# Optimization experiments

Hardware: AMD Instinct MI355X
Metric: run time of the kernel (lower is better)

Reference implementation:

```python
import jax, jax.numpy as jnp
import numpy as np

B, N, C = 16, 2048, 384
CLUSTER_NUM = 512
K_NN = 5


def setup_inputs() -> dict:
    key = jax.random.key(0)
    k1, k2, k3, k4 = jax.random.split(key, 4)
    x = jax.random.normal(k1, (B, N, C), dtype=jnp.float32)
    idx_token = jax.random.randint(k2, (B, N), 0, N)
    agg_weight = jnp.ones((B, N, 1), dtype=jnp.float32)
    density_noise = jax.random.uniform(k3, (B, N), dtype=jnp.float32)
    score_w = jax.random.normal(k4, (1, C), dtype=jnp.float32) * 0.02
    score_b = jnp.zeros((1,), dtype=jnp.float32)
    return {"x": x, "idx_token": idx_token, "agg_weight": agg_weight,
            "density_noise": density_noise, "score_w": score_w, "score_b": score_b}


def _cluster_dpc_knn(x, density_noise, cluster_num, k):
    # x: [B,N,C]; clustering is done under no_grad in the original
    x = jax.lax.stop_gradient(x)
    b, n, c = x.shape
    sq = jnp.sum(x * x, axis=-1)  # [B,N]
    d2 = sq[:, :, None] + sq[:, None, :] - 2.0 * jnp.einsum('bnc,bmc->bnm', x, x)
    dist = jnp.sqrt(jnp.maximum(d2, 0.0)) / (c ** 0.5)  # [B,N,N] cdist/sqrt(C)
    # k smallest distances per row
    neg_near, _ = jax.lax.top_k(-dist, k)                # [B,N,k]
    density = jnp.exp(-jnp.mean(neg_near * neg_near, axis=-1))  # [B,N]
    density = density + density_noise * 1e-6             # tie-break noise
    mask = (density[:, None, :] > density[:, :, None]).astype(x.dtype)  # [B,N,N]
    dist_max = jnp.max(dist.reshape(b, -1), axis=-1)[:, None, None]
    dmin = jnp.min(dist * mask + dist_max * (1.0 - mask), axis=-1)  # [B,N]
    score = dmin * density
    _, index_down = jax.lax.top_k(score, cluster_num)    # [B,K] cluster centers
    dist_sub = jnp.take_along_axis(dist, index_down[:, :, None], axis=1)  # [B,K,N]
    idx_cluster = jnp.argmin(dist_sub, axis=1)           # [B,N]
    bi = jnp.arange(b)[:, None]
    centers = jnp.broadcast_to(jnp.arange(cluster_num)[None, :], (b, cluster_num))
    idx_cluster = idx_cluster.at[bi, index_down].set(centers)
    return idx_cluster, index_down


def reference(x, idx_token, agg_weight, density_noise, score_w, score_b):
    b, n, c = x.shape
    kc = CLUSTER_NUM
    # token score -> weight (equal_weight=False)
    token_weight = jnp.exp(x @ score_w.T + score_b)      # [B,N,1]
    idx_cluster, _ = _cluster_dpc_knn(x, density_noise, kc, K_NN)
    # merge tokens via segment sums
    bi = jnp.arange(b)[:, None]
    idx = (idx_cluster + bi * kc).reshape(-1)            # [B*N]
    all_weight = jax.ops.segment_sum(token_weight.reshape(-1, 1), idx,
                                     num_segments=b * kc) + 1e-6  # [B*K,1]
    norm_weight = token_weight / all_weight[idx].reshape(b, n, 1)
    x_merged = jax.ops.segment_sum((x * norm_weight).reshape(-1, c), idx,
                                   num_segments=b * kc).reshape(b, kc, c)
    idx_token_new = jnp.take_along_axis(idx_cluster, idx_token, axis=1)  # [B,N]
    weight_t = jnp.take_along_axis(norm_weight, idx_token[:, :, None], axis=1)
    agg_weight_new = agg_weight * weight_t               # [B,N,1]
    return x_merged, idx_token_new, agg_weight_new
```

## Files before the change

### kernel.cpp

```cpp
#include <hip/hip_runtime.h>
#include <math.h>

static constexpr int BB  = 16;
static constexpr int NN  = 2048;
static constexpr int CC  = 384;
static constexpr int KCL = 512;
static constexpr float RSQC = 0.051031036307982884f;

typedef short  bf16x8 __attribute__((ext_vector_type(8)));
typedef float  f32x4  __attribute__((ext_vector_type(4)));

__device__ __forceinline__ unsigned short f2b(float v) {
    unsigned u = __float_as_uint(v);
    unsigned r = (u + 0x7FFFu + ((u >> 16) & 1u)) >> 16;
    return (unsigned short)r;
}
__device__ __forceinline__ float b2f(unsigned short b) {
    return __uint_as_float(((unsigned)b) << 16);
}

__device__ __forceinline__ void gload16(const void* g, void* l) {
    __builtin_amdgcn_global_load_lds(
        (const __attribute__((address_space(1))) void*)g,
        (__attribute__((address_space(3))) void*)l, 16, 0, 0);
}

__global__ __launch_bounds__(256) void k_prep(
    const float* __restrict__ x, const float* __restrict__ sw,
    const float* __restrict__ sb, float* __restrict__ sq, float* __restrict__ tw,
    unsigned short* __restrict__ Xh, unsigned short* __restrict__ Xl)
{
    int row  = blockIdx.x * 4 + (threadIdx.x >> 6);
    int lane = threadIdx.x & 63;
    const float* xr = x + (size_t)row * CC;
    unsigned short* xh = Xh + (size_t)row * CC;
    unsigned short* xl = Xl + (size_t)row * CC;
    float s2 = 0.f, sd = 0.f;
    for (int c = lane; c < CC; c += 64) {
        float v = xr[c];
        s2 += v * v;
        sd += v * sw[c];
        unsigned short h = f2b(v);
        xh[c] = h;
        xl[c] = f2b(v - b2f(h));
    }
    #pragma unroll
    for (int o = 32; o > 0; o >>= 1) {
        s2 += __shfl_down(s2, o);
        sd += __shfl_down(sd, o);
    }
    if (lane == 0) {
        sq[row] = s2;
        tw[row] = expf(sd + sb[0]);
    }
}

__global__ __launch_bounds__(256) void k_rowstats(
    const float* __restrict__ x, const float* __restrict__ sw,
    const float* __restrict__ sb, float* __restrict__ sq, float* __restrict__ tw)
{
    int row  = blockIdx.x * 4 + (threadIdx.x >> 6);
    int lane = threadIdx.x & 63;
    const float* xr = x + (size_t)row * CC;
    float s2 = 0.f, sd = 0.f;
    for (int c = lane; c < CC; c += 64) {
        float v = xr[c];
        s2 += v * v;
        sd += v * sw[c];
    }
    #pragma unroll
    for (int o = 32; o > 0; o >>= 1) {
        s2 += __shfl_down(s2, o);
        sd += __shfl_down(sd, o);
    }
    if (lane == 0) {
        sq[row] = s2;
        tw[row] = expf(sd + sb[0]);
    }
}


__global__ __launch_bounds__(256) void k_gemm_sym(
    const unsigned short* __restrict__ Xh, const unsigned short* __restrict__ Xl,
    const float* __restrict__ sq, float* __restrict__ D, int b0)
{
    const int b = b0 + blockIdx.z;
    int q = blockIdx.x;
    int ti = 0;
    while (q >= (16 - ti)) { q -= (16 - ti); ++ti; }
    const int tj = ti + q;
    const int i0 = ti * 128, j0 = tj * 128;

    const unsigned short* Xhb = Xh + (size_t)b * NN * CC;
    const unsigned short* Xlb = Xl + (size_t)b * NN * CC;
    const float* sqb = sq + b * NN;
    float* Db = D + (size_t)blockIdx.z * NN * NN;

    __shared__ union {
        unsigned short u16[4][128][32];
        float tr[64][129];
    } sm;

    const int t  = threadIdx.x;
    const int w  = t >> 6;
    const int l  = t & 63;
    const int wr = w >> 1, wc = w & 1;
    const int lt = l & 15, sl = l >> 4;

    f32x4 acc[4][4];
    #pragma unroll
    for (int fr = 0; fr < 4; ++fr)
        #pragma unroll
        for (int fc = 0; fc < 4; ++fc) acc[fr][fc] = (f32x4)0.0f;

    for (int kc = 0; kc < CC; kc += 32) {
        #pragma unroll
        for (int p = 0; p < 4; ++p) {
            const unsigned short* src = (p == 0) ? Xhb : (p == 1) ? Xlb
                                      : (p == 2) ? Xhb : Xlb;
            const int base0 = (p < 2) ? i0 : j0;
            #pragma unroll
            for (int u = 0; u < 2; ++u) {
                int seg = w * 2 + u;
                int r   = seg * 16 + (l >> 2);
                int s   = (l & 3) ^ ((r >> 1) & 3);
                gload16(src + (size_t)(base0 + r) * CC + kc + s * 8,
                        &sm.u16[p][seg * 16][0]);
            }
        }
        __syncthreads();

        bf16x8 fah[4], fal[4], fbh[4], fbl[4];
        #pragma unroll
        for (int fr = 0; fr < 4; ++fr) {
            int ra = wr * 64 + fr * 16 + lt;
            int sa = (sl ^ ((ra >> 1) & 3)) * 8;
            fah[fr] = *(const bf16x8*)&sm.u16[0][ra][sa];
            fal[fr] = *(const bf16x8*)&sm.u16[1][ra][sa];
        }
        #pragma unroll
        for (int fc = 0; fc < 4; ++fc) {
            int rb = wc * 64 + fc * 16 + lt;
            int sb_ = (sl ^ ((rb >> 1) & 3)) * 8;
            fbh[fc] = *(const bf16x8*)&sm.u16[2][rb][sb_];
            fbl[fc] = *(const bf16x8*)&sm.u16[3][rb][sb_];
        }
        #pragma unroll
        for (int fr = 0; fr < 4; ++fr)
            #pragma unroll
            for (int fc = 0; fc < 4; ++fc) {
                acc[fr][fc] = __builtin_amdgcn_mfma_f32_16x16x32_bf16(
                    fah[fr], fbh[fc], acc[fr][fc], 0, 0, 0);
                acc[fr][fc] = __builtin_amdgcn_mfma_f32_16x16x32_bf16(
                    fah[fr], fbl[fc], acc[fr][fc], 0, 0, 0);
                acc[fr][fc] = __builtin_amdgcn_mfma_f32_16x16x32_bf16(
                    fal[fr], fbh[fc], acc[fr][fc], 0, 0, 0);
            }
        __syncthreads();
    }

    float sqr[4][4], sqc[4];
    #pragma unroll
    for (int fr = 0; fr < 4; ++fr)
        #pragma unroll
        for (int reg = 0; reg < 4; ++reg)
            sqr[fr][reg] = sqb[i0 + wr * 64 + fr * 16 + sl * 4 + reg];
    #pragma unroll
    for (int fc = 0; fc < 4; ++fc)
        sqc[fc] = sqb[j0 + wc * 64 + fc * 16 + lt];

    #pragma unroll
    for (int fr = 0; fr < 4; ++fr)
        #pragma unroll
        for (int fc = 0; fc < 4; ++fc)
            #pragma unroll
            for (int reg = 0; reg < 4; ++reg) {
                int row = i0 + wr * 64 + fr * 16 + sl * 4 + reg;
                int col = j0 + wc * 64 + fc * 16 + lt;
                float d2 = fmaxf(sqr[fr][reg] + sqc[fc] - 2.0f * acc[fr][fc][reg], 0.0f);
                Db[(size_t)row * NN + col] = d2;
            }

    if (ti != tj) {
        #pragma unroll
        for (int h = 0; h < 2; ++h) {
            __syncthreads();
            if (wr == h) {
                #pragma unroll
                for (int fr = 0; fr < 4; ++fr)
                    #pragma unroll
                    for (int fc = 0; fc < 4; ++fc)
                        #pragma unroll
                        for (int reg = 0; reg < 4; ++reg) {
                            int rl = fr * 16 + sl * 4 + reg;
                            int cl = wc * 64 + fc * 16 + lt;
                            float d2 = fmaxf(sqr[fr][reg] + sqc[fc]
                                             - 2.0f * acc[fr][fc][reg], 0.0f);
                            sm.tr[rl][cl] = d2;
                        }
            }
            __syncthreads();
            for (int idx = t; idx < 128 * 64; idx += 256) {
                int c  = idx >> 6;
                int rl = idx & 63;
                Db[(size_t)(j0 + c) * NN + i0 + h * 64 + rl] = sm.tr[rl][c];
            }
        }
    }
}

__global__ __launch_bounds__(256) void k_density2(
    const float* __restrict__ D, const float* __restrict__ noise,
    float* __restrict__ dens, float* __restrict__ rowmax)
{
    int gid  = blockIdx.x * 4 + (threadIdx.x >> 6);
    int lane = threadIdx.x & 63;
    const float* row = D + (size_t)gid * NN;
    float t5[5] = {1e30f, 1e30f, 1e30f, 1e30f, 1e30f};
    float mx = 0.f;
    auto ins5 = [&](float v) {
        if (v < t5[4]) {
            t5[4] = v;
            #pragma unroll
            for (int q = 4; q > 0; --q) {
                if (t5[q] < t5[q - 1]) { float tmp = t5[q - 1]; t5[q - 1] = t5[q]; t5[q] = tmp; }
            }
        }
    };
    #pragma unroll
    for (int it = 0; it < 8; ++it) {
        float4 v = ((const float4*)row)[it * 64 + lane];
        mx = fmaxf(mx, fmaxf(fmaxf(v.x, v.y), fmaxf(v.z, v.w)));
        ins5(v.x); ins5(v.y); ins5(v.z); ins5(v.w);
    }
    #pragma unroll
    for (int o = 1; o < 64; o <<= 1) {
        float b0 = __shfl_xor(t5[0], o), b1 = __shfl_xor(t5[1], o);
        float b2 = __shfl_xor(t5[2], o), b3 = __shfl_xor(t5[3], o);
        float b4 = __shfl_xor(t5[4], o);
        mx = fmaxf(mx, __shfl_xor(mx, o));
        ins5(b0); ins5(b1); ins5(b2); ins5(b3); ins5(b4);
    }
    if (lane == 0) {
        float m2 = (t5[0] + t5[1] + t5[2] + t5[3] + t5[4]) * (1.0f / (5.0f * CC));
        dens[gid]   = expf(-m2) + noise[gid] * 1e-6f;
        rowmax[gid] = mx;
    }
}

__global__ __launch_bounds__(256) void k_distmax2(
    const float* __restrict__ rowmax, float* __restrict__ dmax)
{
    int b = blockIdx.x, t = threadIdx.x;
    float m = 0.f;
    for (int i = t; i < NN; i += 256) m = fmaxf(m, rowmax[b * NN + i]);
    __shared__ float red[256];
    red[t] = m; __syncthreads();
    for (int o = 128; o > 0; o >>= 1) {
        if (t < o) red[t] = fmaxf(red[t], red[t + o]);
        __syncthreads();
    }
    if (t == 0) dmax[b] = sqrtf(red[0]) * RSQC;
}

__global__ __launch_bounds__(256) void k_dmin2(
    const float* __restrict__ D, const float* __restrict__ dens,
    const float* __restrict__ dmax, float* __restrict__ score)
{
    int gid  = blockIdx.x * 4 + (threadIdx.x >> 6);
    int lane = threadIdx.x & 63;
    int bl   = gid >> 11;
    const float* row = D + (size_t)gid * NN;
    const float* dn  = dens + (size_t)bl * NN;
    float di = dens[gid];
    float m = 1e30f;
    #pragma unroll
    for (int it = 0; it < 8; ++it) {
        float4 v = ((const float4*)row)[it * 64 + lane];
        float4 dj = ((const float4*)dn)[it * 64 + lane];
        if (dj.x > di) m = fminf(m, v.x);
        if (dj.y > di) m = fminf(m, v.y);
        if (dj.z > di) m = fminf(m, v.z);
        if (dj.w > di) m = fminf(m, v.w);
    }
    #pragma unroll
    for (int o = 32; o > 0; o >>= 1) m = fminf(m, __shfl_down(m, o));
    if (lane == 0) {
        float dm = fminf(sqrtf(m) * RSQC, dmax[bl]);
        score[gid] = dm * di;
    }
}

__global__ __launch_bounds__(256) void k_assign2(
    const float* __restrict__ D, const int* __restrict__ idown,
    int* __restrict__ idxc)
{
    int bl = blockIdx.y;
    int tl = threadIdx.x & 63;
    int g  = threadIdx.x >> 6;
    int n  = blockIdx.x * 64 + tl;
    const float* Db = D + (size_t)bl * NN * NN;
    const int* idb  = idown + bl * KCL;
    float best = 1e30f; int bk = 0;
    for (int k = g * 128; k < (g + 1) * 128; ++k) {
        float v = Db[(size_t)idb[k] * NN + n];
        if (v < best) { best = v; bk = k; }
    }
    __shared__ float bvs[4][64];
    __shared__ int   bks[4][64];
    bvs[g][tl] = best; bks[g][tl] = bk;
    __syncthreads();
    if (threadIdx.x < 64) {
        float bv = bvs[0][threadIdx.x]; int bkk = bks[0][threadIdx.x];
        #pragma unroll
        for (int gg = 1; gg < 4; ++gg) {
            if (bvs[gg][threadIdx.x] < bv) { bv = bvs[gg][threadIdx.x]; bkk = bks[gg][threadIdx.x]; }
        }
        idxc[bl * NN + blockIdx.x * 64 + threadIdx.x] = bkk;
    }
}


__global__ __launch_bounds__(256) void k_density(
    const float* __restrict__ x, const float* __restrict__ sq,
    const float* __restrict__ noise, float* __restrict__ dens,
    float* __restrict__ rowmax)
{
    const int b  = blockIdx.y;
    const int i0 = blockIdx.x * 64;
    const float* xb  = x + (size_t)b * NN * CC;
    const float* sqb = sq + b * NN;
    __shared__ float As[16][64];
    __shared__ float Bs[16][64];
    __shared__ float mrg[64][16][5];
    __shared__ float mrgmax[64][16];
    const int t  = threadIdx.x;
    const int tx = t & 15, ty = t >> 4;
    const int lr = t >> 2, lk4 = (t & 3) * 4;

    float top[4][5];
    float rmax[4];
    float sqi[4];
    #pragma unroll
    for (int r = 0; r < 4; ++r) {
        sqi[r]  = sqb[i0 + ty * 4 + r];
        rmax[r] = 0.f;
        #pragma unroll
        for (int q = 0; q < 5; ++q) top[r][q] = 1e30f;
    }

    for (int j0 = 0; j0 < NN; j0 += 64) {
        float acc[4][4];
        #pragma unroll
        for (int r = 0; r < 4; ++r)
            #pragma unroll
            for (int s = 0; s < 4; ++s) acc[r][s] = 0.f;

        for (int k0 = 0; k0 < CC; k0 += 16) {
            float4 av = *(const float4*)(xb + (size_t)(i0 + lr) * CC + k0 + lk4);
            float4 bv = *(const float4*)(xb + (size_t)(j0 + lr) * CC + k0 + lk4);
            As[lk4 + 0][lr] = av.x; As[lk4 + 1][lr] = av.y;
            As[lk4 + 2][lr] = av.z; As[lk4 + 3][lr] = av.w;
            Bs[lk4 + 0][lr] = bv.x; Bs[lk4 + 1][lr] = bv.y;
            Bs[lk4 + 2][lr] = bv.z; Bs[lk4 + 3][lr] = bv.w;
            __syncthreads();
            #pragma unroll
            for (int kk = 0; kk < 16; ++kk) {
                float4 a4 = *(const float4*)&As[kk][ty * 4];
                float4 b4 = *(const float4*)&Bs[kk][tx * 4];
                float ar[4] = {a4.x, a4.y, a4.z, a4.w};
                float br[4] = {b4.x, b4.y, b4.z, b4.w};
                #pragma unroll
                for (int r = 0; r < 4; ++r)
                    #pragma unroll
                    for (int s = 0; s < 4; ++s)
                        acc[r][s] = fmaf(ar[r], br[s], acc[r][s]);
            }
            __syncthreads();
        }
        float sqj[4];
        #pragma unroll
        for (int s = 0; s < 4; ++s) sqj[s] = sqb[j0 + tx * 4 + s];
        #pragma unroll
        for (int r = 0; r < 4; ++r) {
            #pragma unroll
            for (int s = 0; s < 4; ++s) {
                float d2 = sqi[r] + sqj[s] - 2.0f * acc[r][s];
                float d  = sqrtf(fmaxf(d2, 0.0f)) * RSQC;
                rmax[r] = fmaxf(rmax[r], d);
                if (d < top[r][4]) {
                    top[r][4] = d;
                    #pragma unroll
                    for (int q = 4; q > 0; --q) {
                        if (top[r][q] < top[r][q - 1]) {
                            float tmp = top[r][q - 1];
                            top[r][q - 1] = top[r][q];
                            top[r][q] = tmp;
                        }
                    }
                }
            }
        }
    }
    #pragma unroll
    for (int r = 0; r < 4; ++r) {
        #pragma unroll
        for (int q = 0; q < 5; ++q) mrg[ty * 4 + r][tx][q] = top[r][q];
        mrgmax[ty * 4 + r][tx] = rmax[r];
    }
    __syncthreads();
    if (t < 64) {
        float t5[5] = {1e30f, 1e30f, 1e30f, 1e30f, 1e30f};
        float mx = 0.f;
        for (int c = 0; c < 16; ++c) {
            mx = fmaxf(mx, mrgmax[t][c]);
            #pragma unroll
            for (int q = 0; q < 5; ++q) {
                float d = mrg[t][c][q];
                if (d < t5[4]) {
                    t5[4] = d;
                    #pragma unroll
                    for (int u = 4; u > 0; --u) {
                        if (t5[u] < t5[u - 1]) {
                            float tmp = t5[u - 1]; t5[u - 1] = t5[u]; t5[u] = tmp;
                        }
                    }
                }
            }
        }
        float m2 = (t5[0]*t5[0] + t5[1]*t5[1] + t5[2]*t5[2] +
                    t5[3]*t5[3] + t5[4]*t5[4]) / 5.0f;
        int i = i0 + t;
        dens[b * NN + i]   = expf(-m2) + noise[b * NN + i] * 1e-6f;
        rowmax[b * NN + i] = mx;
    }
}

__global__ __launch_bounds__(256) void k_distmax(
    const float* __restrict__ rowmax, float* __restrict__ dmax)
{
    int b = blockIdx.x, t = threadIdx.x;
    float m = 0.f;
    for (int i = t; i < NN; i += 256) m = fmaxf(m, rowmax[b * NN + i]);
    __shared__ float red[256];
    red[t] = m; __syncthreads();
    for (int o = 128; o > 0; o >>= 1) {
        if (t < o) red[t] = fmaxf(red[t], red[t + o]);
        __syncthreads();
    }
    if (t == 0) dmax[b] = red[0];
}

__global__ __launch_bounds__(256) void k_dmin(
    const float* __restrict__ x, const float* __restrict__ sq,
    const float* __restrict__ dens, const float* __restrict__ dmax,
    float* __restrict__ score)
{
    const int b  = blockIdx.y;
    const int i0 = blockIdx.x * 64;
    const float* xb  = x + (size_t)b * NN * CC;
    const float* sqb = sq + b * NN;
    const float* dnb = dens + b * NN;
    __shared__ float As[16][64];
    __shared__ float Bs[16][64];
    __shared__ float mrgmin[64][16];
    const int t  = threadIdx.x;
    const int tx = t & 15, ty = t >> 4;
    const int lr = t >> 2, lk4 = (t & 3) * 4;

    float sqi[4], di[4], mn[4];
    #pragma unroll
    for (int r = 0; r < 4; ++r) {
        sqi[r] = sqb[i0 + ty * 4 + r];
        di[r]  = dnb[i0 + ty * 4 + r];
        mn[r]  = 1e30f;
    }

    for (int j0 = 0; j0 < NN; j0 += 64) {
        float acc[4][4];
        #pragma unroll
        for (int r = 0; r < 4; ++r)
            #pragma unroll
            for (int s = 0; s < 4; ++s) acc[r][s] = 0.f;

        for (int k0 = 0; k0 < CC; k0 += 16) {
            float4 av = *(const float4*)(xb + (size_t)(i0 + lr) * CC + k0 + lk4);
            float4 bv = *(const float4*)(xb + (size_t)(j0 + lr) * CC + k0 + lk4);
            As[lk4 + 0][lr] = av.x; As[lk4 + 1][lr] = av.y;
            As[lk4 + 2][lr] = av.z; As[lk4 + 3][lr] = av.w;
            Bs[lk4 + 0][lr] = bv.x; Bs[lk4 + 1][lr] = bv.y;
            Bs[lk4 + 2][lr] = bv.z; Bs[lk4 + 3][lr] = bv.w;
            __syncthreads();
            #pragma unroll
            for (int kk = 0; kk < 16; ++kk) {
                float4 a4 = *(const float4*)&As[kk][ty * 4];
                float4 b4 = *(const float4*)&Bs[kk][tx * 4];
                float ar[4] = {a4.x, a4.y, a4.z, a4.w};
                float br[4] = {b4.x, b4.y, b4.z, b4.w};
                #pragma unroll
                for (int r = 0; r < 4; ++r)
                    #pragma unroll
                    for (int s = 0; s < 4; ++s)
                        acc[r][s] = fmaf(ar[r], br[s], acc[r][s]);
            }
            __syncthreads();
        }
        float dj[4];
        #pragma unroll
        for (int s = 0; s < 4; ++s) dj[s] = dnb[j0 + tx * 4 + s];
        float sqj[4];
        #pragma unroll
        for (int s = 0; s < 4; ++s) sqj[s] = sqb[j0 + tx * 4 + s];
        #pragma unroll
        for (int r = 0; r < 4; ++r) {
            #pragma unroll
            for (int s = 0; s < 4; ++s) {
                float d2 = sqi[r] + sqj[s] - 2.0f * acc[r][s];
                float d  = sqrtf(fmaxf(d2, 0.0f)) * RSQC;
                if (dj[s] > di[r]) mn[r] = fminf(mn[r], d);
            }
        }
    }
    #pragma unroll
    for (int r = 0; r < 4; ++r) mrgmin[ty * 4 + r][tx] = mn[r];
    __syncthreads();
    if (t < 64) {
        float m = 1e30f;
        for (int c = 0; c < 16; ++c) m = fminf(m, mrgmin[t][c]);
        float dm = fminf(dmax[b], m);
        score[b * NN + i0 + t] = dm * dnb[i0 + t];
    }
}

__global__ __launch_bounds__(256) void k_assign(
    const float* __restrict__ x, const float* __restrict__ sq,
    const int* __restrict__ idown, int* __restrict__ idxc)
{
    const int b  = blockIdx.y;
    const int n0 = blockIdx.x * 64;
    const float* xb  = x + (size_t)b * NN * CC;
    const float* sqb = sq + b * NN;
    const int* idb = idown + b * KCL;
    __shared__ float As[16][64];
    __shared__ float Bs[16][64];
    __shared__ float mv[64][16];
    __shared__ int   mk[64][16];
    const int t  = threadIdx.x;
    const int tx = t & 15, ty = t >> 4;
    const int lr = t >> 2, lk4 = (t & 3) * 4;

    float sqt[4];
    #pragma unroll
    for (int s = 0; s < 4; ++s) sqt[s] = sqb[n0 + tx * 4 + s];
    float bestv[4] = {1e30f, 1e30f, 1e30f, 1e30f};
    int   bestk[4] = {0, 0, 0, 0};

    for (int c0 = 0; c0 < KCL; c0 += 64) {
        int crow = idb[c0 + lr];
        float acc[4][4];
        #pragma unroll
        for (int r = 0; r < 4; ++r)
            #pragma unroll
            for (int s = 0; s < 4; ++s) acc[r][s] = 0.f;

        for (int k0 = 0; k0 < CC; k0 += 16) {
            float4 av = *(const float4*)(xb + (size_t)crow * CC + k0 + lk4);
            float4 bv = *(const float4*)(xb + (size_t)(n0 + lr) * CC + k0 + lk4);
            As[lk4 + 0][lr] = av.x; As[lk4 + 1][lr] = av.y;
            As[lk4 + 2][lr] = av.z; As[lk4 + 3][lr] = av.w;
            Bs[lk4 + 0][lr] = bv.x; Bs[lk4 + 1][lr] = bv.y;
            Bs[lk4 + 2][lr] = bv.z; Bs[lk4 + 3][lr] = bv.w;
            __syncthreads();
            #pragma unroll
            for (int kk = 0; kk < 16; ++kk) {
                float4 a4 = *(const float4*)&As[kk][ty * 4];
                float4 b4 = *(const float4*)&Bs[kk][tx * 4];
                float ar[4] = {a4.x, a4.y, a4.z, a4.w};
                float br[4] = {b4.x, b4.y, b4.z, b4.w};
                #pragma unroll
                for (int r = 0; r < 4; ++r)
                    #pragma unroll
                    for (int s = 0; s < 4; ++s)
                        acc[r][s] = fmaf(ar[r], br[s], acc[r][s]);
            }
            __syncthreads();
        }
        float sqc[4];
        #pragma unroll
        for (int r = 0; r < 4; ++r) sqc[r] = sqb[idb[c0 + ty * 4 + r]];
        #pragma unroll
        for (int r = 0; r < 4; ++r) {
            int kg = c0 + ty * 4 + r;
            #pragma unroll
            for (int s = 0; s < 4; ++s) {
                float e = fmaxf(sqc[r] + sqt[s] - 2.0f * acc[r][s], 0.0f);
                if (e < bestv[s]) { bestv[s] = e; bestk[s] = kg; }
            }
        }
    }
    #pragma unroll
    for (int s = 0; s < 4; ++s) {
        mv[tx * 4 + s][ty] = bestv[s];
        mk[tx * 4 + s][ty] = bestk[s];
    }
    __syncthreads();
    if (t < 64) {
        float bv = 1e30f; int bk = 1 << 30;
        for (int c = 0; c < 16; ++c) {
            float v = mv[t][c]; int k = mk[t][c];
            if (v < bv || (v == bv && k < bk)) { bv = v; bk = k; }
        }
        idxc[b * NN + n0 + t] = bk;
    }
}


__global__ __launch_bounds__(1024) void k_topk(
    const float* __restrict__ score, int* __restrict__ idown)
{
    int b = blockIdx.x, t = threadIdx.x;
    __shared__ float s[NN];
    __shared__ int   si[NN];
    s[t]         = score[b * NN + t];        si[t]        = t;
    s[t + 1024]  = score[b * NN + t + 1024]; si[t + 1024] = t + 1024;
    __syncthreads();
    for (int k = 2; k <= NN; k <<= 1) {
        for (int j = k >> 1; j > 0; j >>= 1) {
            int i = (t & (j - 1)) | ((t & ~(j - 1)) << 1);
            int l = i | j;
            bool dir = ((i & k) == 0);
            float svi = s[i], svl = s[l];
            int   ii  = si[i], il = si[l];
            bool before_l_i = (svl > svi) || (svl == svi && il < ii);
            if (before_l_i == dir) {
                s[i] = svl; s[l] = svi;
                si[i] = il; si[l] = ii;
            }
            __syncthreads();
        }
    }
    if (t < KCL) idown[b * KCL + t] = si[t];
}

__global__ __launch_bounds__(256) void k_override(
    const int* __restrict__ idown, int* __restrict__ idxc)
{
    int g = blockIdx.x * 256 + threadIdx.x;
    int b = g >> 9, k = g & 511;
    idxc[b * NN + idown[g]] = k;
}

__global__ __launch_bounds__(512) void k_merge(
    const float* __restrict__ x, const float* __restrict__ tw,
    const int* __restrict__ idxc, float* __restrict__ aw, float* __restrict__ xm)
{
    int b = blockIdx.y, k = blockIdx.x;
    __shared__ int members[NN];
    __shared__ int wc[8];
    __shared__ float red[512];
    int t = threadIdx.x, lane = t & 63, w = t >> 6;
    const int* ib = idxc + b * NN;
    int base = 0;
    for (int r0 = 0; r0 < NN; r0 += 512) {
        int n = r0 + t;
        bool m = (ib[n] == k);
        unsigned long long msk = __ballot(m);
        if (lane == 0) wc[w] = __popcll(msk);
        __syncthreads();
        int off = 0;
        for (int ww = 0; ww < w; ++ww) off += wc[ww];
        int tot = 0;
        #pragma unroll
        for (int ww = 0; ww < 8; ++ww) tot += wc[ww];
        if (m) members[base + off + __popcll(msk & ((1ull << lane) - 1ull))] = n;
        base += tot;
        __syncthreads();
    }
    int cnt = base;
    const float* twb = tw + b * NN;
    float ps = 0.f;
    for (int p = t; p < cnt; p += 512) ps += twb[members[p]];
    red[t] = ps; __syncthreads();
    for (int o = 256; o > 0; o >>= 1) {
        if (t < o) red[t] += red[t + o];
        __syncthreads();
    }
    float awf = red[0] + 1e-6f;
    if (t == 0) aw[b * KCL + k] = awf;
    if (t < CC) {
        const float* xb = x + (size_t)b * NN * CC;
        float s = 0.f;
        for (int p = 0; p < cnt; ++p) {
            int n = members[p];
            s += xb[(size_t)n * CC + t] * twb[n];
        }
        xm[((size_t)b * KCL + k) * CC + t] = s / awf;
    }
}

__global__ __launch_bounds__(256) void k_out(
    const int* __restrict__ idx_token, const float* __restrict__ aggw,
    const float* __restrict__ tw, const float* __restrict__ aw,
    const int* __restrict__ idxc, float* __restrict__ out_idx,
    float* __restrict__ out_agg)
{
    int g = blockIdx.x * 256 + threadIdx.x;
    int b = g >> 11;
    int it = idx_token[g];
    int kclu = idxc[b * NN + it];
    out_idx[g] = (float)kclu;
    float nw = tw[b * NN + it] / aw[b * KCL + kclu];
    out_agg[g] = aggw[g] * nw;
}

extern "C" void kernel_launch(void* const* d_in, const int* in_sizes, int n_in,
                              void* d_out, int out_size, void* d_ws, size_t ws_size,
                              hipStream_t stream) {
    const float* x         = (const float*)d_in[0];
    const int*   idx_token = (const int*)  d_in[1];
    const float* aggw      = (const float*)d_in[2];
    const float* noise     = (const float*)d_in[3];
    const float* sw        = (const float*)d_in[4];
    const float* sb        = (const float*)d_in[5];

    float* ws      = (float*)d_ws;
    float* sq      = ws;
    float* tw      = ws + 32768;
    float* dens    = ws + 65536;
    float* rowmax  = ws + 98304;
    float* score   = ws + 131072;
    float* dmax    = ws + 163840;
    float* aw      = ws + 163904;
    int*   idown   = (int*)(ws + 172096);
    int*   idxc    = (int*)(ws + 180288);

    unsigned short* Xh = (unsigned short*)(ws + 213056);
    unsigned short* Xl = (unsigned short*)(ws + 213056 + 6291456);
    float* Dbuf        = ws + 213056 + 2 * 6291456;

    const size_t head_bytes = (size_t)(213056 + 2 * 6291456) * 4;
    size_t avail = (ws_size > head_bytes) ? (ws_size - head_bytes) : 0;
    int nbg = 0;
    for (int g = 16; g >= 1; g >>= 1) {
        if ((size_t)g * NN * NN * 4 <= avail) { nbg = g; break; }
    }

    float* xm      = (float*)d_out;
    float* out_idx = xm + (size_t)BB * KCL * CC;
    float* out_agg = out_idx + (size_t)BB * NN;

    if (nbg >= 16) {
        k_prep    <<<dim3(BB * NN / 4), 256, 0, stream>>>(x, sw, sb, sq, tw, Xh, Xl);
        k_gemm_sym<<<dim3(136, 1, BB), 256, 0, stream>>>(Xh, Xl, sq, Dbuf, 0);
        k_density2<<<dim3(BB * NN / 4), 256, 0, stream>>>(Dbuf, noise, dens, rowmax);
        k_distmax2<<<dim3(BB), 256, 0, stream>>>(rowmax, dmax);
        k_dmin2   <<<dim3(BB * NN / 4), 256, 0, stream>>>(Dbuf, dens, dmax, score);
        k_topk    <<<dim3(BB), 1024, 0, stream>>>(score, idown);
        k_assign2 <<<dim3(NN / 64, BB), 256, 0, stream>>>(Dbuf, idown, idxc);
        k_override<<<dim3(BB * KCL / 256), 256, 0, stream>>>(idown, idxc);
    } else if (nbg >= 1) {
        k_prep<<<dim3(BB * NN / 4), 256, 0, stream>>>(x, sw, sb, sq, tw, Xh, Xl);
        int G = (nbg >= 8) ? 8 : nbg;
        for (int b0 = 0; b0 < BB; b0 += G) {
            int g = (b0 + G <= BB) ? G : (BB - b0);
            k_gemm_sym<<<dim3(136, 1, g), 256, 0, stream>>>(Xh, Xl, sq, Dbuf, b0);
            k_density2<<<dim3(g * NN / 4), 256, 0, stream>>>(Dbuf, noise + b0 * NN,
                                                             dens + b0 * NN, rowmax + b0 * NN);
            k_distmax2<<<dim3(g), 256, 0, stream>>>(rowmax + b0 * NN, dmax + b0);
            k_dmin2   <<<dim3(g * NN / 4), 256, 0, stream>>>(Dbuf, dens + b0 * NN,
                                                             dmax + b0, score + b0 * NN);
            k_topk    <<<dim3(g), 1024, 0, stream>>>(score + b0 * NN, idown + b0 * KCL);
            k_assign2 <<<dim3(NN / 64, g), 256, 0, stream>>>(Dbuf, idown + b0 * KCL,
                                                             idxc + b0 * NN);
            k_override<<<dim3(g * KCL / 256), 256, 0, stream>>>(idown + b0 * KCL,
                                                                idxc + b0 * NN);
        }
    } else {
        k_rowstats<<<dim3(BB * NN / 4), 256, 0, stream>>>(x, sw, sb, sq, tw);
        k_density <<<dim3(NN / 64, BB), 256, 0, stream>>>(x, sq, noise, dens, rowmax);
        k_distmax <<<dim3(BB), 256, 0, stream>>>(rowmax, dmax);
        k_dmin    <<<dim3(NN / 64, BB), 256, 0, stream>>>(x, sq, dens, dmax, score);
        k_topk    <<<dim3(BB), 1024, 0, stream>>>(score, idown);
        k_assign  <<<dim3(NN / 64, BB), 256, 0, stream>>>(x, sq, idown, idxc);
        k_override<<<dim3(BB * KCL / 256), 256, 0, stream>>>(idown, idxc);
    }

    k_merge<<<dim3(KCL, BB), 512, 0, stream>>>(x, tw, idxc, aw, xm);
    k_out  <<<dim3(BB * NN / 256), 256, 0, stream>>>(idx_token, aggw, tw, aw, idxc,
                                                     out_idx, out_agg);
}
```

Baseline: 445.5 us.

## Fuse density top-5 and row max into symmetric distance GEMM epilogue

The GEMM epilogue now computes per-tile partial top-5 smallest distances and row/column maxima, writing them to a small partial buffer. A lighter density kernel then merges 16 tile partials instead of rescanning the full NxN distance matrix, and it atomically reduces the global distance max, removing a separate max kernel. The override kernel is folded into assign through an inverse-index map built in top-k. The change also adds nontemporal stores for D and a workgroup remap across batches. This trades extra epilogue work and shuffles in the GEMM for one fewer full pass over D.

```diff
diff --git a/kernel.cpp b/kernel.cpp
--- a/kernel.cpp
+++ b/kernel.cpp
@@ -18,18 +18,28 @@
 __device__ __forceinline__ float b2f(unsigned short b) {
     return __uint_as_float(((unsigned)b) << 16);
 }
-
 __device__ __forceinline__ void gload16(const void* g, void* l) {
     __builtin_amdgcn_global_load_lds(
         (const __attribute__((address_space(1))) void*)g,
         (__attribute__((address_space(3))) void*)l, 16, 0, 0);
 }
+__device__ __forceinline__ void ins5(float* t5, float v) {
+    if (v < t5[4]) {
+        t5[4] = v;
+        #pragma unroll
+        for (int q = 4; q > 0; --q) {
+            if (t5[q] < t5[q - 1]) { float tmp = t5[q - 1]; t5[q - 1] = t5[q]; t5[q] = tmp; }
+        }
+    }
+}
 
 __global__ __launch_bounds__(256) void k_prep(
     const float* __restrict__ x, const float* __restrict__ sw,
     const float* __restrict__ sb, float* __restrict__ sq, float* __restrict__ tw,
-    unsigned short* __restrict__ Xh, unsigned short* __restrict__ Xl)
-{
+    unsigned short* __restrict__ Xh, unsigned short* __restrict__ Xl,
+    unsigned* __restrict__ dmaxraw)
+{
+    if (blockIdx.x == 0 && threadIdx.x < 64) dmaxraw[threadIdx.x] = 0u;
     int row  = blockIdx.x * 4 + (threadIdx.x >> 6);
     int lane = threadIdx.x & 63;
     const float* xr = x + (size_t)row * CC;
@@ -82,10 +92,15 @@
 
 __global__ __launch_bounds__(256) void k_gemm_sym(
     const unsigned short* __restrict__ Xh, const unsigned short* __restrict__ Xl,
-    const float* __restrict__ sq, float* __restrict__ D, int b0)
-{
-    const int b = b0 + blockIdx.z;
-    int q = blockIdx.x;
+    const float* __restrict__ sq, float* __restrict__ D, float* __restrict__ P,
+    int b0)
+{
+    int f   = blockIdx.x + 136 * blockIdx.z;
+    int nwg = 136 * gridDim.z;
+    int wg  = ((nwg & 7) == 0) ? ((f & 7) * (nwg >> 3) + (f >> 3)) : f;
+    int bz  = wg / 136;
+    int q   = wg % 136;
+    const int b = b0 + bz;
     int ti = 0;
     while (q >= (16 - ti)) { q -= (16 - ti); ++ti; }
     const int tj = ti + q;
@@ -94,11 +109,12 @@
     const unsigned short* Xhb = Xh + (size_t)b * NN * CC;
     const unsigned short* Xlb = Xl + (size_t)b * NN * CC;
     const float* sqb = sq + b * NN;
-    float* Db = D + (size_t)blockIdx.z * NN * NN;
+    float* Db = D + (size_t)bz * NN * NN;
 
     __shared__ union {
         unsigned short u16[4][128][32];
         float tr[64][129];
+        float part[2][128][8];
     } sm;
 
     const int t  = threadIdx.x;
@@ -178,10 +194,98 @@
                 int row = i0 + wr * 64 + fr * 16 + sl * 4 + reg;
                 int col = j0 + wc * 64 + fc * 16 + lt;
                 float d2 = fmaxf(sqr[fr][reg] + sqc[fc] - 2.0f * acc[fr][fc][reg], 0.0f);
-                Db[(size_t)row * NN + col] = d2;
-            }
+                __builtin_nontemporal_store(d2, Db + (size_t)row * NN + col);
+            }
+
+    #pragma unroll
+    for (int fr = 0; fr < 4; ++fr) {
+        #pragma unroll
+        for (int reg = 0; reg < 4; ++reg) {
+            float t5[5] = {1e30f, 1e30f, 1e30f, 1e30f, 1e30f};
+            float rmx = 0.f;
+            #pragma unroll
+            for (int fc = 0; fc < 4; ++fc) {
+                float d2 = fmaxf(sqr[fr][reg] + sqc[fc] - 2.0f * acc[fr][fc][reg], 0.0f);
+                rmx = fmaxf(rmx, d2);
+                ins5(t5, d2);
+            }
+            #pragma unroll
+            for (int mk = 1; mk <= 8; mk <<= 1) {
+                float o0 = __shfl_xor(t5[0], mk), o1 = __shfl_xor(t5[1], mk);
+                float o2 = __shfl_xor(t5[2], mk), o3 = __shfl_xor(t5[3], mk);
+                float o4 = __shfl_xor(t5[4], mk);
+                rmx = fmaxf(rmx, __shfl_xor(rmx, mk));
+                ins5(t5, o0); ins5(t5, o1); ins5(t5, o2); ins5(t5, o3); ins5(t5, o4);
+            }
+            if (lt == 0) {
+                int rl = wr * 64 + fr * 16 + sl * 4 + reg;
+                sm.part[wc][rl][0] = t5[0]; sm.part[wc][rl][1] = t5[1];
+                sm.part[wc][rl][2] = t5[2]; sm.part[wc][rl][3] = t5[3];
+                sm.part[wc][rl][4] = t5[4]; sm.part[wc][rl][5] = rmx;
+            }
+        }
+    }
+    __syncthreads();
+    if (t < 128) {
+        float t5[5]; float rmx;
+        #pragma unroll
+        for (int qq = 0; qq < 5; ++qq) t5[qq] = sm.part[0][t][qq];
+        rmx = sm.part[0][t][5];
+        #pragma unroll
+        for (int qq = 0; qq < 5; ++qq) ins5(t5, sm.part[1][t][qq]);
+        rmx = fmaxf(rmx, sm.part[1][t][5]);
+        float* dst = P + ((size_t)(b * 16 + tj) * NN + (i0 + t)) * 8;
+        float4 o0 = {t5[0], t5[1], t5[2], t5[3]};
+        float4 o1 = {t5[4], rmx, 0.f, 0.f};
+        *(float4*)dst = o0;
+        *(float4*)(dst + 4) = o1;
+    }
 
     if (ti != tj) {
+        __syncthreads();
+        #pragma unroll
+        for (int fc = 0; fc < 4; ++fc) {
+            float t5[5] = {1e30f, 1e30f, 1e30f, 1e30f, 1e30f};
+            float cmx = 0.f;
+            #pragma unroll
+            for (int fr = 0; fr < 4; ++fr)
+                #pragma unroll
+                for (int reg = 0; reg < 4; ++reg) {
+                    float d2 = fmaxf(sqr[fr][reg] + sqc[fc] - 2.0f * acc[fr][fc][reg], 0.0f);
+                    cmx = fmaxf(cmx, d2);
+                    ins5(t5, d2);
+                }
+            #pragma unroll
+            for (int mk = 16; mk <= 32; mk <<= 1) {
+                float o0 = __shfl_xor(t5[0], mk), o1 = __shfl_xor(t5[1], mk);
+                float o2 = __shfl_xor(t5[2], mk), o3 = __shfl_xor(t5[3], mk);
+                float o4 = __shfl_xor(t5[4], mk);
+                cmx = fmaxf(cmx, __shfl_xor(cmx, mk));
+                ins5(t5, o0); ins5(t5, o1); ins5(t5, o2); ins5(t5, o3); ins5(t5, o4);
+            }
+            if (sl == 0) {
+                int cl = wc * 64 + fc * 16 + lt;
+                sm.part[wr][cl][0] = t5[0]; sm.part[wr][cl][1] = t5[1];
+                sm.part[wr][cl][2] = t5[2]; sm.part[wr][cl][3] = t5[3];
+                sm.part[wr][cl][4] = t5[4]; sm.part[wr][cl][5] = cmx;
+            }
+        }
+        __syncthreads();
+        if (t < 128) {
+            float t5[5]; float cmx;
+            #pragma unroll
+            for (int qq = 0; qq < 5; ++qq) t5[qq] = sm.part[0][t][qq];
+            cmx = sm.part[0][t][5];
+            #pragma unroll
+            for (int qq = 0; qq < 5; ++qq) ins5(t5, sm.part[1][t][qq]);
+            cmx = fmaxf(cmx, sm.part[1][t][5]);
+            float* dst = P + ((size_t)(b * 16 + ti) * NN + (j0 + t)) * 8;
+            float4 o0 = {t5[0], t5[1], t5[2], t5[3]};
+            float4 o1 = {t5[4], cmx, 0.f, 0.f};
+            *(float4*)dst = o0;
+            *(float4*)(dst + 4) = o1;
+        }
+
         #pragma unroll
         for (int h = 0; h < 2; ++h) {
             __syncthreads();
@@ -203,69 +307,44 @@
             for (int idx = t; idx < 128 * 64; idx += 256) {
                 int c  = idx >> 6;
                 int rl = idx & 63;
-                Db[(size_t)(j0 + c) * NN + i0 + h * 64 + rl] = sm.tr[rl][c];
-            }
-        }
-    }
-}
-
-__global__ __launch_bounds__(256) void k_density2(
-    const float* __restrict__ D, const float* __restrict__ noise,
-    float* __restrict__ dens, float* __restrict__ rowmax)
-{
-    int gid  = blockIdx.x * 4 + (threadIdx.x >> 6);
-    int lane = threadIdx.x & 63;
-    const float* row = D + (size_t)gid * NN;
+                __builtin_nontemporal_store(sm.tr[rl][c],
+                    Db + (size_t)(j0 + c) * NN + i0 + h * 64 + rl);
+            }
+        }
+    }
+}
+
+__global__ __launch_bounds__(256) void k_density3(
+    const float* __restrict__ P, const float* __restrict__ noise,
+    float* __restrict__ dens, unsigned* __restrict__ dmaxraw)
+{
+    int gid = blockIdx.x * 256 + threadIdx.x;
+    int b   = gid >> 11;
+    int n   = gid & 2047;
+    const float* p = P + ((size_t)(b * 16) * NN + n) * 8;
     float t5[5] = {1e30f, 1e30f, 1e30f, 1e30f, 1e30f};
     float mx = 0.f;
-    auto ins5 = [&](float v) {
-        if (v < t5[4]) {
-            t5[4] = v;
-            #pragma unroll
-            for (int q = 4; q > 0; --q) {
-                if (t5[q] < t5[q - 1]) { float tmp = t5[q - 1]; t5[q - 1] = t5[q]; t5[q] = tmp; }
-            }
-        }
-    };
-    #pragma unroll
-    for (int it = 0; it < 8; ++it) {
-        float4 v = ((const float4*)row)[it * 64 + lane];
-        mx = fmaxf(mx, fmaxf(fmaxf(v.x, v.y), fmaxf(v.z, v.w)));
-        ins5(v.x); ins5(v.y); ins5(v.z); ins5(v.w);
-    }
-    #pragma unroll
-    for (int o = 1; o < 64; o <<= 1) {
-        float b0 = __shfl_xor(t5[0], o), b1 = __shfl_xor(t5[1], o);
-        float b2 = __shfl_xor(t5[2], o), b3 = __shfl_xor(t5[3], o);
-        float b4 = __shfl_xor(t5[4], o);
-        mx = fmaxf(mx, __shfl_xor(mx, o));
-        ins5(b0); ins5(b1); ins5(b2); ins5(b3); ins5(b4);
-    }
-    if (lane == 0) {
-        float m2 = (t5[0] + t5[1] + t5[2] + t5[3] + t5[4]) * (1.0f / (5.0f * CC));
-        dens[gid]   = expf(-m2) + noise[gid] * 1e-6f;
-        rowmax[gid] = mx;
-    }
-}
-
-__global__ __launch_bounds__(256) void k_distmax2(
-    const float* __restrict__ rowmax, float* __restrict__ dmax)
-{
-    int b = blockIdx.x, t = threadIdx.x;
-    float m = 0.f;
-    for (int i = t; i < NN; i += 256) m = fmaxf(m, rowmax[b * NN + i]);
+    #pragma unroll
+    for (int tc = 0; tc < 16; ++tc) {
+        float4 a = *(const float4*)(p + (size_t)tc * NN * 8);
+        float4 c = *(const float4*)(p + (size_t)tc * NN * 8 + 4);
+        ins5(t5, a.x); ins5(t5, a.y); ins5(t5, a.z); ins5(t5, a.w); ins5(t5, c.x);
+        mx = fmaxf(mx, c.y);
+    }
+    float m2 = (t5[0] + t5[1] + t5[2] + t5[3] + t5[4]) * (1.0f / (5.0f * CC));
+    dens[gid] = expf(-m2) + noise[gid] * 1e-6f;
     __shared__ float red[256];
-    red[t] = m; __syncthreads();
+    red[threadIdx.x] = mx; __syncthreads();
     for (int o = 128; o > 0; o >>= 1) {
-        if (t < o) red[t] = fmaxf(red[t], red[t + o]);
+        if (threadIdx.x < o) red[threadIdx.x] = fmaxf(red[threadIdx.x], red[threadIdx.x + o]);
         __syncthreads();
     }
-    if (t == 0) dmax[b] = sqrtf(red[0]) * RSQC;
+    if (threadIdx.x == 0) atomicMax(&dmaxraw[b], __float_as_uint(red[0]));
 }
 
 __global__ __launch_bounds__(256) void k_dmin2(
     const float* __restrict__ D, const float* __restrict__ dens,
-    const float* __restrict__ dmax, float* __restrict__ score)
+    const unsigned* __restrict__ dmaxraw, float* __restrict__ score)
 {
     int gid  = blockIdx.x * 4 + (threadIdx.x >> 6);
     int lane = threadIdx.x & 63;
@@ -276,7 +355,7 @@
     float m = 1e30f;
     #pragma unroll
     for (int it = 0; it < 8; ++it) {
-        float4 v = ((const float4*)row)[it * 64 + lane];
+        float4 v  = ((const float4*)row)[it * 64 + lane];
         float4 dj = ((const float4*)dn)[it * 64 + lane];
         if (dj.x > di) m = fminf(m, v.x);
         if (dj.y > di) m = fminf(m, v.y);
@@ -286,14 +365,15 @@
     #pragma unroll
     for (int o = 32; o > 0; o >>= 1) m = fminf(m, __shfl_down(m, o));
     if (lane == 0) {
-        float dm = fminf(sqrtf(m) * RSQC, dmax[bl]);
+        float dmv = sqrtf(__uint_as_float(dmaxraw[bl])) * RSQC;
+        float dm = fminf(sqrtf(m) * RSQC, dmv);
         score[gid] = dm * di;
     }
 }
 
 __global__ __launch_bounds__(256) void k_assign2(
     const float* __restrict__ D, const int* __restrict__ idown,
-    int* __restrict__ idxc)
+    const int* __restrict__ invc, int* __restrict__ idxc)
 {
     int bl = blockIdx.y;
     int tl = threadIdx.x & 63;
@@ -316,7 +396,9 @@
         for (int gg = 1; gg < 4; ++gg) {
             if (bvs[gg][threadIdx.x] < bv) { bv = bvs[gg][threadIdx.x]; bkk = bks[gg][threadIdx.x]; }
         }
-        idxc[bl * NN + blockIdx.x * 64 + threadIdx.x] = bkk;
+        int nn = blockIdx.x * 64 + threadIdx.x;
+        int iv = invc[bl * NN + nn];
+        idxc[bl * NN + nn] = (iv >= 0) ? iv : bkk;
     }
 }
 
@@ -415,18 +497,7 @@
         for (int c = 0; c < 16; ++c) {
             mx = fmaxf(mx, mrgmax[t][c]);
             #pragma unroll
-            for (int q = 0; q < 5; ++q) {
-                float d = mrg[t][c][q];
-                if (d < t5[4]) {
-                    t5[4] = d;
-                    #pragma unroll
-                    for (int u = 4; u > 0; --u) {
-                        if (t5[u] < t5[u - 1]) {
-                            float tmp = t5[u - 1]; t5[u - 1] = t5[u]; t5[u] = tmp;
-                        }
-                    }
-                }
-            }
+            for (int q = 0; q < 5; ++q) ins5(t5, mrg[t][c][q]);
         }
         float m2 = (t5[0]*t5[0] + t5[1]*t5[1] + t5[2]*t5[2] +
                     t5[3]*t5[3] + t5[4]*t5[4]) / 5.0f;
@@ -614,9 +685,17 @@
     }
 }
 
+__global__ __launch_bounds__(256) void k_override(
+    const int* __restrict__ idown, int* __restrict__ idxc)
+{
+    int g = blockIdx.x * 256 + threadIdx.x;
+    int b = g >> 9, k = g & 511;
+    idxc[b * NN + idown[g]] = k;
+}
+
 
 __global__ __launch_bounds__(1024) void k_topk(
-    const float* __restrict__ score, int* __restrict__ idown)
+    const float* __restrict__ score, int* __restrict__ idown, int* __restrict__ invc)
 {
     int b = blockIdx.x, t = threadIdx.x;
     __shared__ float s[NN];
@@ -640,14 +719,10 @@
         }
     }
     if (t < KCL) idown[b * KCL + t] = si[t];
-}
-
-__global__ __launch_bounds__(256) void k_override(
-    const int* __restrict__ idown, int* __restrict__ idxc)
-{
-    int g = blockIdx.x * 256 + threadIdx.x;
-    int b = g >> 9, k = g & 511;
-    idxc[b * NN + idown[g]] = k;
+    invc[b * NN + t] = -1;
+    invc[b * NN + t + 1024] = -1;
+    __syncthreads();
+    if (t < KCL) invc[b * NN + si[t]] = t;
 }
 
 __global__ __launch_bounds__(512) void k_merge(
@@ -729,16 +804,19 @@
     float* dens    = ws + 65536;
     float* rowmax  = ws + 98304;
     float* score   = ws + 131072;
-    float* dmax    = ws + 163840;
+    unsigned* dmaxraw = (unsigned*)(ws + 163840);
     float* aw      = ws + 163904;
     int*   idown   = (int*)(ws + 172096);
     int*   idxc    = (int*)(ws + 180288);
-
-    unsigned short* Xh = (unsigned short*)(ws + 213056);
-    unsigned short* Xl = (unsigned short*)(ws + 213056 + 6291456);
-    float* Dbuf        = ws + 213056 + 2 * 6291456;
-
-    const size_t head_bytes = (size_t)(213056 + 2 * 6291456) * 4;
+    int*   invc    = (int*)(ws + 213056);
+
+    unsigned short* Xh = (unsigned short*)(ws + 245824);
+    unsigned short* Xl = (unsigned short*)(ws + 245824 + 6291456);
+    float* Pbuf        = ws + 245824 + 2 * 6291456;
+    float* Dbuf        = Pbuf + (size_t)BB * 16 * NN * 8;
+
+    const size_t head_floats = 245824 + 2 * 6291456 + (size_t)BB * 16 * NN * 8;
+    const size_t head_bytes  = head_floats * 4;
     size_t avail = (ws_size > head_bytes) ? (ws_size - head_bytes) : 0;
     int nbg = 0;
     for (int g = 16; g >= 1; g >>= 1) {
@@ -749,38 +827,27 @@
     float* out_idx = xm + (size_t)BB * KCL * CC;
     float* out_agg = out_idx + (size_t)BB * NN;
 
-    if (nbg >= 16) {
-        k_prep    <<<dim3(BB * NN / 4), 256, 0, stream>>>(x, sw, sb, sq, tw, Xh, Xl);
-        k_gemm_sym<<<dim3(136, 1, BB), 256, 0, stream>>>(Xh, Xl, sq, Dbuf, 0);
-        k_density2<<<dim3(BB * NN / 4), 256, 0, stream>>>(Dbuf, noise, dens, rowmax);
-        k_distmax2<<<dim3(BB), 256, 0, stream>>>(rowmax, dmax);
-        k_dmin2   <<<dim3(BB * NN / 4), 256, 0, stream>>>(Dbuf, dens, dmax, score);
-        k_topk    <<<dim3(BB), 1024, 0, stream>>>(score, idown);
-        k_assign2 <<<dim3(NN / 64, BB), 256, 0, stream>>>(Dbuf, idown, idxc);
-        k_override<<<dim3(BB * KCL / 256), 256, 0, stream>>>(idown, idxc);
-    } else if (nbg >= 1) {
-        k_prep<<<dim3(BB * NN / 4), 256, 0, stream>>>(x, sw, sb, sq, tw, Xh, Xl);
-        int G = (nbg >= 8) ? 8 : nbg;
+    if (nbg >= 1) {
+        k_prep<<<dim3(BB * NN / 4), 256, 0, stream>>>(x, sw, sb, sq, tw, Xh, Xl, dmaxraw);
+        int G = (nbg >= 16) ? 16 : nbg;
         for (int b0 = 0; b0 < BB; b0 += G) {
-            int g = (b0 + G <= BB) ? G : (BB - b0);
-            k_gemm_sym<<<dim3(136, 1, g), 256, 0, stream>>>(Xh, Xl, sq, Dbuf, b0);
-            k_density2<<<dim3(g * NN / 4), 256, 0, stream>>>(Dbuf, noise + b0 * NN,
-                                                             dens + b0 * NN, rowmax + b0 * NN);
-            k_distmax2<<<dim3(g), 256, 0, stream>>>(rowmax + b0 * NN, dmax + b0);
-            k_dmin2   <<<dim3(g * NN / 4), 256, 0, stream>>>(Dbuf, dens + b0 * NN,
-                                                             dmax + b0, score + b0 * NN);
-            k_topk    <<<dim3(g), 1024, 0, stream>>>(score + b0 * NN, idown + b0 * KCL);
-            k_assign2 <<<dim3(NN / 64, g), 256, 0, stream>>>(Dbuf, idown + b0 * KCL,
-                                                             idxc + b0 * NN);
-            k_override<<<dim3(g * KCL / 256), 256, 0, stream>>>(idown + b0 * KCL,
-                                                                idxc + b0 * NN);
+            k_gemm_sym<<<dim3(136, 1, G), 256, 0, stream>>>(Xh, Xl, sq, Dbuf, Pbuf, b0);
+            k_density3<<<dim3(G * NN / 256), 256, 0, stream>>>(
+                Pbuf + (size_t)b0 * 16 * NN * 8, noise + b0 * NN,
+                dens + b0 * NN, dmaxraw + b0);
+            k_dmin2<<<dim3(G * NN / 4), 256, 0, stream>>>(
+                Dbuf, dens + b0 * NN, dmaxraw + b0, score + b0 * NN);
+            k_topk<<<dim3(G), 1024, 0, stream>>>(
+                score + b0 * NN, idown + b0 * KCL, invc + b0 * NN);
+            k_assign2<<<dim3(NN / 64, G), 256, 0, stream>>>(
+                Dbuf, idown + b0 * KCL, invc + b0 * NN, idxc + b0 * NN);
         }
     } else {
         k_rowstats<<<dim3(BB * NN / 4), 256, 0, stream>>>(x, sw, sb, sq, tw);
         k_density <<<dim3(NN / 64, BB), 256, 0, stream>>>(x, sq, noise, dens, rowmax);
-        k_distmax <<<dim3(BB), 256, 0, stream>>>(rowmax, dmax);
-        k_dmin    <<<dim3(NN / 64, BB), 256, 0, stream>>>(x, sq, dens, dmax, score);
-        k_topk    <<<dim3(BB), 1024, 0, stream>>>(score, idown);
+        k_distmax <<<dim3(BB), 256, 0, stream>>>(rowmax, (float*)dmaxraw);
+        k_dmin    <<<dim3(NN / 64, BB), 256, 0, stream>>>(x, sq, dens, (float*)dmaxraw, score);
+        k_topk    <<<dim3(BB), 1024, 0, stream>>>(score, idown, invc);
         k_assign  <<<dim3(NN / 64, BB), 256, 0, stream>>>(x, sq, idown, idxc);
         k_override<<<dim3(BB * KCL / 256), 256, 0, stream>>>(idown, idxc);
     }
```

Result: slower. 580.6 us (+30.3%).
